# Kernel optimization log

Hardware: AMD Instinct MI355X
Metric: run time of the kernel (lower is better)

Reference implementation:

```python
import jax, jax.numpy as jnp
import numpy as np
import math

B_SZ, N, D, H = 16384, 10, 256, 8
D_H = D // H

def setup_inputs() -> dict:
    key = jax.random.key(0)
    ks = jax.random.split(key, 7)
    s = 1.0 / math.sqrt(D)
    return {
        "Z": jax.random.normal(ks[0], (B_SZ, N, D), dtype=jnp.float32),
        "role_pos_ids": jax.random.randint(ks[1], (B_SZ, N), 0, 10),
        "WQ": jax.random.normal(ks[2], (D, D), dtype=jnp.float32) * s,
        "WK": jax.random.normal(ks[3], (D, D), dtype=jnp.float32) * s,
        "WV": jax.random.normal(ks[4], (D, D), dtype=jnp.float32) * s,
        "WO": jax.random.normal(ks[5], (D, D), dtype=jnp.float32) * s,
        "Bp": jax.random.normal(ks[6], (H, 10, 10), dtype=jnp.float32) * 0.02,
    }

def reference(Z, role_pos_ids, WQ, WK, WV, WO, Bp):
    Bs, n, _ = Z.shape
    # projections -> (B, H, N, d_h)
    q = (Z @ WQ).reshape(Bs, n, H, D_H).transpose(0, 2, 1, 3)
    k = (Z @ WK).reshape(Bs, n, H, D_H).transpose(0, 2, 1, 3)
    v = (Z @ WV).reshape(Bs, n, H, D_H).transpose(0, 2, 1, 3)
    scores = jnp.einsum('bhid,bhjd->bhij', q, k) / math.sqrt(D_H)
    # bias[b,h,i,j] = Bp[h, c[b,i], c[b,j]]  -> advanced indexing gives (H,B,N,N)
    bias = Bp[:, role_pos_ids[:, :, None], role_pos_ids[:, None, :]]
    scores = scores + bias.transpose(1, 0, 2, 3)
    attn = jax.nn.softmax(scores, axis=-1)
    out = jnp.einsum('bhij,bhjd->bhid', attn, v)
    out = out.transpose(0, 2, 1, 3).reshape(Bs, n, D)
    return out @ WO
```

## Files before the change

kernel.cpp:

```cpp
#include <hip/hip_runtime.h>
#include <hip/hip_bf16.h>


typedef __attribute__((ext_vector_type(8))) short bf16x8;
typedef __attribute__((ext_vector_type(4))) float f32x4;

__device__ __forceinline__ unsigned short f2bf(float f) {
  union { __hip_bfloat16 h; unsigned short u; } cv;
  cv.h = __float2bfloat16(f);
  return cv.u;
}
__device__ __forceinline__ float bflo(unsigned int u) { return __uint_as_float(u << 16); }
__device__ __forceinline__ float bfhi(unsigned int u) { return __uint_as_float(u & 0xffff0000u); }

__global__ void prep_wt_kernel(const float* __restrict__ WQ, const float* __restrict__ WK,
                               const float* __restrict__ WV, const float* __restrict__ WO,
                               __hip_bfloat16* __restrict__ wt) {
  const int k = blockIdx.x;
  const int n = threadIdx.x;
  wt[0 * 65536 + n * 256 + k] = __float2bfloat16(WQ[k * 256 + n]);
  wt[1 * 65536 + n * 256 + k] = __float2bfloat16(WK[k * 256 + n]);
  wt[2 * 65536 + n * 256 + k] = __float2bfloat16(WV[k * 256 + n]);
  wt[3 * 65536 + n * 256 + k] = __float2bfloat16(WO[k * 256 + n]);
}

__global__ __launch_bounds__(256) void fused_qkv_attn_kernel(
    const float* __restrict__ Z, const __hip_bfloat16* __restrict__ wt,
    const int* __restrict__ roles, const float* __restrict__ Bp,
    __hip_bfloat16* __restrict__ attn_out, int gb_off)
{
  __shared__ __align__(16) char lds[72960];
  char* As = lds;
  char* Sp = lds + 40960;

  const int t = threadIdx.x;
  const int lane = t & 63;
  const int wv = t >> 6;
  const int g = lane >> 4, cx = lane & 15;
  const int blk = blockIdx.x;
  const size_t r0 = (size_t)blk * 80;

  #pragma unroll
  for (int c = 0; c < 10; ++c) {
    const int idx = c * 256 + t;
    const int row = idx >> 5, ch = idx & 31;
    const float* src = Z + (r0 + row) * 256 + ch * 8;
    float4 f0 = *(const float4*)(src);
    float4 f1 = *(const float4*)(src + 4);
    union { bf16x8 v; unsigned short u[8]; } pk;
    pk.u[0] = f2bf(f0.x); pk.u[1] = f2bf(f0.y);
    pk.u[2] = f2bf(f0.z); pk.u[3] = f2bf(f0.w);
    pk.u[4] = f2bf(f1.x); pk.u[5] = f2bf(f1.y);
    pk.u[6] = f2bf(f1.z); pk.u[7] = f2bf(f1.w);
    *(bf16x8*)(As + row * 512 + ((ch ^ (row & 7)) * 16)) = pk.v;
  }
  __syncthreads();

  #pragma unroll 1
  for (int p = 0; p < 4; ++p) {
    f32x4 acc[5][3];
    #pragma unroll
    for (int mi = 0; mi < 5; ++mi)
      #pragma unroll
      for (int nf = 0; nf < 3; ++nf) acc[mi][nf] = (f32x4){0.f, 0.f, 0.f, 0.f};

    const __hip_bfloat16* bptr[3];
    #pragma unroll
    for (int nf = 0; nf < 3; ++nf) {
      const int f = wv * 3 + nf;
      const int mf = f >> 2;
      const int ncol = p * 64 + (f & 3) * 16;
      bptr[nf] = wt + mf * 65536 + (ncol + cx) * 256 + g * 8;
    }
    #pragma unroll
    for (int kk = 0; kk < 8; ++kk) {
      bf16x8 bfr[3];
      #pragma unroll
      for (int nf = 0; nf < 3; ++nf) bfr[nf] = *(const bf16x8*)(bptr[nf] + kk * 32);
      bf16x8 afr[5];
      #pragma unroll
      for (int mi = 0; mi < 5; ++mi) {
        const int row = mi * 16 + cx;
        const int ch = (kk * 4 + g) ^ (row & 7);
        afr[mi] = *(const bf16x8*)(As + row * 512 + ch * 16);
      }
      #pragma unroll
      for (int mi = 0; mi < 5; ++mi)
        #pragma unroll
        for (int nf = 0; nf < 3; ++nf)
          acc[mi][nf] = __builtin_amdgcn_mfma_f32_16x16x32_bf16(afr[mi], bfr[nf], acc[mi][nf], 0, 0, 0);
    }
    #pragma unroll
    for (int mi = 0; mi < 5; ++mi)
      #pragma unroll
      for (int nf = 0; nf < 3; ++nf)
        #pragma unroll
        for (int jj = 0; jj < 4; ++jj) {
          const int row = mi * 16 + g * 4 + jj;
          const int col = wv * 48 + nf * 16 + cx;
          *(unsigned short*)(Sp + row * 400 + col * 2) = f2bf(acc[mi][nf][jj]);
        }
    __syncthreads();

    if (t < 160) {
      const int b = t / 20;
      const int hh = (t / 10) % 2;
      const int i = t % 10;
      const int h = 2 * p + hh;
      const int gb = gb_off + blk * 8 + b;
      const char* base = Sp + (b * 10) * 400 + hh * 64;

      float qf[32];
      {
        const char* qrow = base + i * 400;
        #pragma unroll
        for (int c = 0; c < 4; ++c) {
          uint4 u = *(const uint4*)(qrow + c * 16);
          qf[c*8+0] = bflo(u.x); qf[c*8+1] = bfhi(u.x);
          qf[c*8+2] = bflo(u.y); qf[c*8+3] = bfhi(u.y);
          qf[c*8+4] = bflo(u.z); qf[c*8+5] = bfhi(u.z);
          qf[c*8+6] = bflo(u.w); qf[c*8+7] = bfhi(u.w);
        }
      }
      const int ri = roles[gb * 10 + i];
      const float* bias_row = Bp + h * 100 + ri * 10;

      float s[10];
      #pragma unroll
      for (int j = 0; j < 10; ++j) {
        const char* krow = base + j * 400 + 128;
        float a = 0.f;
        #pragma unroll
        for (int c = 0; c < 4; ++c) {
          uint4 u = *(const uint4*)(krow + c * 16);
          a += qf[c*8+0]*bflo(u.x) + qf[c*8+1]*bfhi(u.x)
             + qf[c*8+2]*bflo(u.y) + qf[c*8+3]*bfhi(u.y)
             + qf[c*8+4]*bflo(u.z) + qf[c*8+5]*bfhi(u.z)
             + qf[c*8+6]*bflo(u.w) + qf[c*8+7]*bfhi(u.w);
        }
        const int rj = roles[gb * 10 + j];
        s[j] = a * 0.17677669529663687f + bias_row[rj];
      }
      float mx = s[0];
      #pragma unroll
      for (int j = 1; j < 10; ++j) mx = fmaxf(mx, s[j]);
      float pr[10], sum = 0.f;
      #pragma unroll
      for (int j = 0; j < 10; ++j) { pr[j] = expf(s[j] - mx); sum += pr[j]; }
      const float inv = 1.f / sum;

      float o[32];
      #pragma unroll
      for (int d = 0; d < 32; ++d) o[d] = 0.f;
      #pragma unroll
      for (int j = 0; j < 10; ++j) {
        const float pj = pr[j] * inv;
        const char* vrow = base + j * 400 + 256;
        #pragma unroll
        for (int c = 0; c < 4; ++c) {
          uint4 u = *(const uint4*)(vrow + c * 16);
          o[c*8+0] += pj * bflo(u.x); o[c*8+1] += pj * bfhi(u.x);
          o[c*8+2] += pj * bflo(u.y); o[c*8+3] += pj * bfhi(u.y);
          o[c*8+4] += pj * bflo(u.z); o[c*8+5] += pj * bfhi(u.z);
          o[c*8+6] += pj * bflo(u.w); o[c*8+7] += pj * bfhi(u.w);
        }
      }
      uint4* op = (uint4*)(attn_out + (r0 + b * 10 + i) * 256 + h * 32);
      #pragma unroll
      for (int c = 0; c < 4; ++c) {
        uint4 u;
        u.x = (unsigned)f2bf(o[c*8+0]) | ((unsigned)f2bf(o[c*8+1]) << 16);
        u.y = (unsigned)f2bf(o[c*8+2]) | ((unsigned)f2bf(o[c*8+3]) << 16);
        u.z = (unsigned)f2bf(o[c*8+4]) | ((unsigned)f2bf(o[c*8+5]) << 16);
        u.w = (unsigned)f2bf(o[c*8+6]) | ((unsigned)f2bf(o[c*8+7]) << 16);
        op[c] = u;
      }
    }
    __syncthreads();
  }
}

__global__ __launch_bounds__(256) void gemm_wo2_kernel(
    const __hip_bfloat16* __restrict__ A, const __hip_bfloat16* __restrict__ wt,
    float* __restrict__ C)
{
  __shared__ __align__(16) char As2[8192];
  const int t = threadIdx.x;
  const int lane = t & 63;
  const int wv = t >> 6;
  const int g = lane >> 4, cx = lane & 15;
  const size_t m0 = (size_t)blockIdx.x * 64;
  const __hip_bfloat16* WOT = wt + 3 * 65536;

  f32x4 acc[4][4];
  #pragma unroll
  for (int a = 0; a < 4; ++a)
    #pragma unroll
    for (int b = 0; b < 4; ++b) acc[a][b] = (f32x4){0.f, 0.f, 0.f, 0.f};

  #pragma unroll 1
  for (int ks = 0; ks < 4; ++ks) {
    if (ks) __syncthreads();
    #pragma unroll
    for (int c = 0; c < 2; ++c) {
      const int idx = c * 256 + t;
      const int row = idx >> 3, ch = idx & 7;
      uint4 raw = *(const uint4*)(A + (m0 + row) * 256 + ks * 64 + ch * 8);
      *(uint4*)(As2 + row * 128 + ((ch ^ (row & 7)) * 16)) = raw;
    }
    __syncthreads();
    #pragma unroll
    for (int kk = 0; kk < 2; ++kk) {
      bf16x8 bfr[4];
      #pragma unroll
      for (int nf = 0; nf < 4; ++nf) {
        const int n = wv * 64 + nf * 16 + cx;
        bfr[nf] = *(const bf16x8*)(WOT + n * 256 + ks * 64 + kk * 32 + g * 8);
      }
      bf16x8 afr[4];
      #pragma unroll
      for (int mi = 0; mi < 4; ++mi) {
        const int row = mi * 16 + cx;
        const int ch = (kk * 4 + g) ^ (row & 7);
        afr[mi] = *(const bf16x8*)(As2 + row * 128 + ch * 16);
      }
      #pragma unroll
      for (int mi = 0; mi < 4; ++mi)
        #pragma unroll
        for (int nf = 0; nf < 4; ++nf)
          acc[mi][nf] = __builtin_amdgcn_mfma_f32_16x16x32_bf16(afr[mi], bfr[nf], acc[mi][nf], 0, 0, 0);
    }
  }
  #pragma unroll
  for (int mi = 0; mi < 4; ++mi)
    #pragma unroll
    for (int nf = 0; nf < 4; ++nf)
      #pragma unroll
      for (int jj = 0; jj < 4; ++jj) {
        const size_t row = m0 + mi * 16 + g * 4 + jj;
        const int col = wv * 64 + nf * 16 + cx;
        C[row * 256 + col] = acc[mi][nf][jj];
      }
}

extern "C" void kernel_launch(void* const* d_in, const int* in_sizes, int n_in,
                              void* d_out, int out_size, void* d_ws, size_t ws_size,
                              hipStream_t stream)
{
  const float* Z     = (const float*)d_in[0];
  const int*   roles = (const int*)d_in[1];
  const float* WQ    = (const float*)d_in[2];
  const float* WK    = (const float*)d_in[3];
  const float* WV    = (const float*)d_in[4];
  const float* WO    = (const float*)d_in[5];
  const float* Bp    = (const float*)d_in[6];
  float* out = (float*)d_out;

  const long M = 163840;
  char* ws = (char*)d_ws;
  __hip_bfloat16* wt = (__hip_bfloat16*)ws;
  const size_t WT_BYTES = 4u * 256u * 256u * 2u;
  __hip_bfloat16* attn_ws = (__hip_bfloat16*)(ws + WT_BYTES);

  size_t avail = (ws_size > WT_BYTES) ? (ws_size - WT_BYTES) : 0;
  long rows_fit = (long)(avail / 512);
  long chunk = (rows_fit / 320) * 320;
  if (chunk > M) chunk = M;
  if (chunk < 320) chunk = 320;

  prep_wt_kernel<<<256, 256, 0, stream>>>(WQ, WK, WV, WO, wt);

  for (long r0 = 0; r0 < M; r0 += chunk) {
    long rows = M - r0;
    if (rows > chunk) rows = chunk;
    fused_qkv_attn_kernel<<<(int)(rows / 80), 256, 0, stream>>>(
        Z + r0 * 256, wt, roles, Bp, attn_ws, (int)(r0 / 10));
    gemm_wo2_kernel<<<(int)(rows / 64), 256, 0, stream>>>(
        attn_ws, wt, out + r0 * 256);
  }
}
```

Baseline: 252.5 us.

## Fuse output projection into attention kernel and overlap next-head QKV GEMM

Merges the separate WO GEMM into the fused QKV+attention kernel. Each head pair's attention output is written back into LDS and immediately multiplied by its slice of WO into persistent accumulators, so the bf16 attention intermediate never goes to global memory. The next head pair's QKV GEMM is issued before the attention step to overlap MFMA work with the scalar softmax code. Roles and Bp are staged in LDS and the score buffer is XOR-swizzled. The cost is higher register pressure from the extra 5x4 accumulator tile, under a launch bound requesting two blocks per CU with about 76 KB LDS each.

```diff
diff --git a/kernel.cpp b/kernel.cpp
--- a/kernel.cpp
+++ b/kernel.cpp
@@ -24,14 +24,16 @@
   wt[3 * 65536 + n * 256 + k] = __float2bfloat16(WO[k * 256 + n]);
 }
 
-__global__ __launch_bounds__(256) void fused_qkv_attn_kernel(
+__global__ __launch_bounds__(256, 2) void fused_all_kernel(
     const float* __restrict__ Z, const __hip_bfloat16* __restrict__ wt,
     const int* __restrict__ roles, const float* __restrict__ Bp,
-    __hip_bfloat16* __restrict__ attn_out, int gb_off)
+    float* __restrict__ out)
 {
-  __shared__ __align__(16) char lds[72960];
+  __shared__ __align__(16) char lds[76480];
   char* As = lds;
   char* Sp = lds + 40960;
+  int* roles_lds = (int*)(lds + 72960);
+  float* Bp_lds = (float*)(lds + 73280);
 
   const int t = threadIdx.x;
   const int lane = t & 63;
@@ -39,6 +41,9 @@
   const int g = lane >> 4, cx = lane & 15;
   const int blk = blockIdx.x;
   const size_t r0 = (size_t)blk * 80;
+
+  if (t < 80) roles_lds[t] = roles[r0 + t];
+  if (t < 200) ((float4*)Bp_lds)[t] = ((const float4*)Bp)[t];
 
   #pragma unroll
   for (int c = 0; c < 10; ++c) {
@@ -56,14 +61,18 @@
   }
   __syncthreads();
 
-  #pragma unroll 1
-  for (int p = 0; p < 4; ++p) {
-    f32x4 acc[5][3];
+  f32x4 acc_o[5][4];
+  #pragma unroll
+  for (int a = 0; a < 5; ++a)
+    #pragma unroll
+    for (int b = 0; b < 4; ++b) acc_o[a][b] = (f32x4){0.f, 0.f, 0.f, 0.f};
+  f32x4 acc_s[5][3];
+
+  auto gemm_qkv = [&](int p) {
     #pragma unroll
     for (int mi = 0; mi < 5; ++mi)
       #pragma unroll
-      for (int nf = 0; nf < 3; ++nf) acc[mi][nf] = (f32x4){0.f, 0.f, 0.f, 0.f};
-
+      for (int nf = 0; nf < 3; ++nf) acc_s[mi][nf] = (f32x4){0.f, 0.f, 0.f, 0.f};
     const __hip_bfloat16* bptr[3];
     #pragma unroll
     for (int nf = 0; nf < 3; ++nf) {
@@ -88,8 +97,11 @@
       for (int mi = 0; mi < 5; ++mi)
         #pragma unroll
         for (int nf = 0; nf < 3; ++nf)
-          acc[mi][nf] = __builtin_amdgcn_mfma_f32_16x16x32_bf16(afr[mi], bfr[nf], acc[mi][nf], 0, 0, 0);
-    }
+          acc_s[mi][nf] = __builtin_amdgcn_mfma_f32_16x16x32_bf16(afr[mi], bfr[nf], acc_s[mi][nf], 0, 0, 0);
+    }
+  };
+
+  auto epi = [&]() {
     #pragma unroll
     for (int mi = 0; mi < 5; ++mi)
       #pragma unroll
@@ -98,148 +110,125 @@
         for (int jj = 0; jj < 4; ++jj) {
           const int row = mi * 16 + g * 4 + jj;
           const int col = wv * 48 + nf * 16 + cx;
-          *(unsigned short*)(Sp + row * 400 + col * 2) = f2bf(acc[mi][nf][jj]);
+          const int region = col >> 6;
+          const int c = (col >> 3) & 7;
+          *(unsigned short*)(Sp + row * 400 + region * 128 +
+                             ((c ^ (row & 7)) * 16) + (col & 7) * 2) = f2bf(acc_s[mi][nf][jj]);
         }
-    __syncthreads();
-
-    if (t < 160) {
-      const int b = t / 20;
-      const int hh = (t / 10) % 2;
-      const int i = t % 10;
-      const int h = 2 * p + hh;
-      const int gb = gb_off + blk * 8 + b;
-      const char* base = Sp + (b * 10) * 400 + hh * 64;
-
-      float qf[32];
-      {
-        const char* qrow = base + i * 400;
-        #pragma unroll
-        for (int c = 0; c < 4; ++c) {
-          uint4 u = *(const uint4*)(qrow + c * 16);
-          qf[c*8+0] = bflo(u.x); qf[c*8+1] = bfhi(u.x);
-          qf[c*8+2] = bflo(u.y); qf[c*8+3] = bfhi(u.y);
-          qf[c*8+4] = bflo(u.z); qf[c*8+5] = bfhi(u.z);
-          qf[c*8+6] = bflo(u.w); qf[c*8+7] = bfhi(u.w);
-        }
-      }
-      const int ri = roles[gb * 10 + i];
-      const float* bias_row = Bp + h * 100 + ri * 10;
-
-      float s[10];
-      #pragma unroll
-      for (int j = 0; j < 10; ++j) {
-        const char* krow = base + j * 400 + 128;
-        float a = 0.f;
-        #pragma unroll
-        for (int c = 0; c < 4; ++c) {
-          uint4 u = *(const uint4*)(krow + c * 16);
-          a += qf[c*8+0]*bflo(u.x) + qf[c*8+1]*bfhi(u.x)
-             + qf[c*8+2]*bflo(u.y) + qf[c*8+3]*bfhi(u.y)
-             + qf[c*8+4]*bflo(u.z) + qf[c*8+5]*bfhi(u.z)
-             + qf[c*8+6]*bflo(u.w) + qf[c*8+7]*bfhi(u.w);
-        }
-        const int rj = roles[gb * 10 + j];
-        s[j] = a * 0.17677669529663687f + bias_row[rj];
-      }
-      float mx = s[0];
-      #pragma unroll
-      for (int j = 1; j < 10; ++j) mx = fmaxf(mx, s[j]);
-      float pr[10], sum = 0.f;
-      #pragma unroll
-      for (int j = 0; j < 10; ++j) { pr[j] = expf(s[j] - mx); sum += pr[j]; }
-      const float inv = 1.f / sum;
-
-      float o[32];
-      #pragma unroll
-      for (int d = 0; d < 32; ++d) o[d] = 0.f;
-      #pragma unroll
-      for (int j = 0; j < 10; ++j) {
-        const float pj = pr[j] * inv;
-        const char* vrow = base + j * 400 + 256;
-        #pragma unroll
-        for (int c = 0; c < 4; ++c) {
-          uint4 u = *(const uint4*)(vrow + c * 16);
-          o[c*8+0] += pj * bflo(u.x); o[c*8+1] += pj * bfhi(u.x);
-          o[c*8+2] += pj * bflo(u.y); o[c*8+3] += pj * bfhi(u.y);
-          o[c*8+4] += pj * bflo(u.z); o[c*8+5] += pj * bfhi(u.z);
-          o[c*8+6] += pj * bflo(u.w); o[c*8+7] += pj * bfhi(u.w);
-        }
-      }
-      uint4* op = (uint4*)(attn_out + (r0 + b * 10 + i) * 256 + h * 32);
+  };
+
+  auto attn = [&](int p) {
+    const int b = t / 20, hh = (t / 10) % 2, i = t % 10;
+    const int h = p * 2 + hh;
+    const int lrow = b * 10 + i;
+    float qf[32];
+    #pragma unroll
+    for (int c = 0; c < 4; ++c) {
+      uint4 u = *(const uint4*)(Sp + lrow * 400 + (((hh * 4 + c) ^ (lrow & 7)) * 16));
+      qf[c*8+0] = bflo(u.x); qf[c*8+1] = bfhi(u.x);
+      qf[c*8+2] = bflo(u.y); qf[c*8+3] = bfhi(u.y);
+      qf[c*8+4] = bflo(u.z); qf[c*8+5] = bfhi(u.z);
+      qf[c*8+6] = bflo(u.w); qf[c*8+7] = bfhi(u.w);
+    }
+    const int ri = roles_lds[b * 10 + i];
+    const float* brow = Bp_lds + h * 100 + ri * 10;
+    float s[10];
+    #pragma unroll
+    for (int j = 0; j < 10; ++j) {
+      const int kr = b * 10 + j;
+      const char* kbase = Sp + kr * 400 + 128;
+      float a = 0.f;
       #pragma unroll
       for (int c = 0; c < 4; ++c) {
-        uint4 u;
-        u.x = (unsigned)f2bf(o[c*8+0]) | ((unsigned)f2bf(o[c*8+1]) << 16);
-        u.y = (unsigned)f2bf(o[c*8+2]) | ((unsigned)f2bf(o[c*8+3]) << 16);
-        u.z = (unsigned)f2bf(o[c*8+4]) | ((unsigned)f2bf(o[c*8+5]) << 16);
-        u.w = (unsigned)f2bf(o[c*8+6]) | ((unsigned)f2bf(o[c*8+7]) << 16);
-        op[c] = u;
-      }
-    }
-    __syncthreads();
-  }
-}
-
-__global__ __launch_bounds__(256) void gemm_wo2_kernel(
-    const __hip_bfloat16* __restrict__ A, const __hip_bfloat16* __restrict__ wt,
-    float* __restrict__ C)
-{
-  __shared__ __align__(16) char As2[8192];
-  const int t = threadIdx.x;
-  const int lane = t & 63;
-  const int wv = t >> 6;
-  const int g = lane >> 4, cx = lane & 15;
-  const size_t m0 = (size_t)blockIdx.x * 64;
-  const __hip_bfloat16* WOT = wt + 3 * 65536;
-
-  f32x4 acc[4][4];
-  #pragma unroll
-  for (int a = 0; a < 4; ++a)
-    #pragma unroll
-    for (int b = 0; b < 4; ++b) acc[a][b] = (f32x4){0.f, 0.f, 0.f, 0.f};
-
-  #pragma unroll 1
-  for (int ks = 0; ks < 4; ++ks) {
-    if (ks) __syncthreads();
-    #pragma unroll
-    for (int c = 0; c < 2; ++c) {
-      const int idx = c * 256 + t;
-      const int row = idx >> 3, ch = idx & 7;
-      uint4 raw = *(const uint4*)(A + (m0 + row) * 256 + ks * 64 + ch * 8);
-      *(uint4*)(As2 + row * 128 + ((ch ^ (row & 7)) * 16)) = raw;
-    }
-    __syncthreads();
+        uint4 u = *(const uint4*)(kbase + (((hh * 4 + c) ^ (kr & 7)) * 16));
+        a += qf[c*8+0]*bflo(u.x) + qf[c*8+1]*bfhi(u.x)
+           + qf[c*8+2]*bflo(u.y) + qf[c*8+3]*bfhi(u.y)
+           + qf[c*8+4]*bflo(u.z) + qf[c*8+5]*bfhi(u.z)
+           + qf[c*8+6]*bflo(u.w) + qf[c*8+7]*bfhi(u.w);
+      }
+      s[j] = a * 0.17677669529663687f + brow[roles_lds[b * 10 + j]];
+    }
+    float mx = s[0];
+    #pragma unroll
+    for (int j = 1; j < 10; ++j) mx = fmaxf(mx, s[j]);
+    float pr[10], sum = 0.f;
+    #pragma unroll
+    for (int j = 0; j < 10; ++j) { pr[j] = expf(s[j] - mx); sum += pr[j]; }
+    const float inv = 1.f / sum;
+    float o[32];
+    #pragma unroll
+    for (int d = 0; d < 32; ++d) o[d] = 0.f;
+    #pragma unroll
+    for (int j = 0; j < 10; ++j) {
+      const float pj = pr[j] * inv;
+      const int kr = b * 10 + j;
+      const char* vbase = Sp + kr * 400 + 256;
+      #pragma unroll
+      for (int c = 0; c < 4; ++c) {
+        uint4 u = *(const uint4*)(vbase + (((hh * 4 + c) ^ (kr & 7)) * 16));
+        o[c*8+0] += pj * bflo(u.x); o[c*8+1] += pj * bfhi(u.x);
+        o[c*8+2] += pj * bflo(u.y); o[c*8+3] += pj * bfhi(u.y);
+        o[c*8+4] += pj * bflo(u.z); o[c*8+5] += pj * bfhi(u.z);
+        o[c*8+6] += pj * bflo(u.w); o[c*8+7] += pj * bfhi(u.w);
+      }
+    }
+    #pragma unroll
+    for (int c = 0; c < 4; ++c) {
+      uint4 u;
+      u.x = (unsigned)f2bf(o[c*8+0]) | ((unsigned)f2bf(o[c*8+1]) << 16);
+      u.y = (unsigned)f2bf(o[c*8+2]) | ((unsigned)f2bf(o[c*8+3]) << 16);
+      u.z = (unsigned)f2bf(o[c*8+4]) | ((unsigned)f2bf(o[c*8+5]) << 16);
+      u.w = (unsigned)f2bf(o[c*8+6]) | ((unsigned)f2bf(o[c*8+7]) << 16);
+      *(uint4*)(Sp + lrow * 400 + (((hh * 4 + c) ^ (lrow & 7)) * 16)) = u;
+    }
+  };
+
+  auto wo = [&](int p) {
+    const __hip_bfloat16* WOT = wt + 3 * 65536;
     #pragma unroll
     for (int kk = 0; kk < 2; ++kk) {
-      bf16x8 bfr[4];
+      bf16x8 bw[4];
       #pragma unroll
       for (int nf = 0; nf < 4; ++nf) {
         const int n = wv * 64 + nf * 16 + cx;
-        bfr[nf] = *(const bf16x8*)(WOT + n * 256 + ks * 64 + kk * 32 + g * 8);
-      }
-      bf16x8 afr[4];
-      #pragma unroll
-      for (int mi = 0; mi < 4; ++mi) {
+        bw[nf] = *(const bf16x8*)(WOT + n * 256 + p * 64 + kk * 32 + g * 8);
+      }
+      bf16x8 aw[5];
+      #pragma unroll
+      for (int mi = 0; mi < 5; ++mi) {
         const int row = mi * 16 + cx;
         const int ch = (kk * 4 + g) ^ (row & 7);
-        afr[mi] = *(const bf16x8*)(As2 + row * 128 + ch * 16);
-      }
-      #pragma unroll
-      for (int mi = 0; mi < 4; ++mi)
+        aw[mi] = *(const bf16x8*)(Sp + row * 400 + ch * 16);
+      }
+      #pragma unroll
+      for (int mi = 0; mi < 5; ++mi)
         #pragma unroll
         for (int nf = 0; nf < 4; ++nf)
-          acc[mi][nf] = __builtin_amdgcn_mfma_f32_16x16x32_bf16(afr[mi], bfr[nf], acc[mi][nf], 0, 0, 0);
-    }
+          acc_o[mi][nf] = __builtin_amdgcn_mfma_f32_16x16x32_bf16(aw[mi], bw[nf], acc_o[mi][nf], 0, 0, 0);
+    }
+  };
+
+  gemm_qkv(0);
+  #pragma unroll 1
+  for (int p = 0; p < 4; ++p) {
+    __syncthreads();
+    epi();
+    __syncthreads();
+    if (p < 3) gemm_qkv(p + 1);
+    if (t < 160) attn(p);
+    __syncthreads();
+    wo(p);
   }
+
   #pragma unroll
-  for (int mi = 0; mi < 4; ++mi)
+  for (int mi = 0; mi < 5; ++mi)
     #pragma unroll
     for (int nf = 0; nf < 4; ++nf)
       #pragma unroll
       for (int jj = 0; jj < 4; ++jj) {
-        const size_t row = m0 + mi * 16 + g * 4 + jj;
+        const size_t row = r0 + mi * 16 + g * 4 + jj;
         const int col = wv * 64 + nf * 16 + cx;
-        C[row * 256 + col] = acc[mi][nf][jj];
+        out[row * 256 + col] = acc_o[mi][nf][jj];
       }
 }
 
@@ -256,26 +245,8 @@
   const float* Bp    = (const float*)d_in[6];
   float* out = (float*)d_out;
 
-  const long M = 163840;
-  char* ws = (char*)d_ws;
-  __hip_bfloat16* wt = (__hip_bfloat16*)ws;
-  const size_t WT_BYTES = 4u * 256u * 256u * 2u;
-  __hip_bfloat16* attn_ws = (__hip_bfloat16*)(ws + WT_BYTES);
-
-  size_t avail = (ws_size > WT_BYTES) ? (ws_size - WT_BYTES) : 0;
-  long rows_fit = (long)(avail / 512);
-  long chunk = (rows_fit / 320) * 320;
-  if (chunk > M) chunk = M;
-  if (chunk < 320) chunk = 320;
+  __hip_bfloat16* wt = (__hip_bfloat16*)d_ws;
 
   prep_wt_kernel<<<256, 256, 0, stream>>>(WQ, WK, WV, WO, wt);
-
-  for (long r0 = 0; r0 < M; r0 += chunk) {
-    long rows = M - r0;
-    if (rows > chunk) rows = chunk;
-    fused_qkv_attn_kernel<<<(int)(rows / 80), 256, 0, stream>>>(
-        Z + r0 * 256, wt, roles, Bp, attn_ws, (int)(r0 / 10));
-    gemm_wo2_kernel<<<(int)(rows / 64), 256, 0, stream>>>(
-        attn_ws, wt, out + r0 * 256);
-  }
-}
+  fused_all_kernel<<<2048, 256, 0, stream>>>(Z, wt, roles, Bp, out);
+}
```

After: 439.9 us. +74.2%, slower.

## Halve attention block tile to 40 rows and swizzle QKV staging in LDS

Applied to the files above, without the earlier changes.

Each fused QKV+attention block now handles 4 batches (40 rows) instead of 8. This shrinks LDS from about 72KB to about 40KB, so with launch_bounds(256,4) more blocks can be resident per CU. The QKV staging buffer gets an XOR-swizzled layout to reduce bank conflicts, and roles are cached in LDS. Softmax uses __expf. The cost is that the 48-row MFMA tiling wastes rows 40-47, which read uninitialized LDS but are discarded, and per-row weight fetches double since each block reloads the weight fragments for half as many rows.

```diff
diff --git a/kernel.cpp b/kernel.cpp
--- a/kernel.cpp
+++ b/kernel.cpp
@@ -24,27 +24,32 @@
   wt[3 * 65536 + n * 256 + k] = __float2bfloat16(WO[k * 256 + n]);
 }
 
-__global__ __launch_bounds__(256) void fused_qkv_attn_kernel(
+#define AS_OFF 0
+#define SP_OFF 24576
+#define RL_OFF 40576
+#define LDS_SZ 40624
+
+__global__ __launch_bounds__(256, 4) void fused_qkv_attn_kernel(
     const float* __restrict__ Z, const __hip_bfloat16* __restrict__ wt,
     const int* __restrict__ roles, const float* __restrict__ Bp,
-    __hip_bfloat16* __restrict__ attn_out, int gb_off)
+    __hip_bfloat16* __restrict__ attn_out)
 {
-  __shared__ __align__(16) char lds[72960];
-  char* As = lds;
-  char* Sp = lds + 40960;
+  __shared__ __align__(16) char lds[LDS_SZ];
+  unsigned char* rl = (unsigned char*)(lds + RL_OFF);
 
   const int t = threadIdx.x;
   const int lane = t & 63;
   const int wv = t >> 6;
   const int g = lane >> 4, cx = lane & 15;
   const int blk = blockIdx.x;
-  const size_t r0 = (size_t)blk * 80;
-
+  const size_t c0 = (size_t)blk * 40;
+
+  if (t < 48) rl[t] = (t < 40) ? (unsigned char)roles[c0 + t] : 0;
   #pragma unroll
-  for (int c = 0; c < 10; ++c) {
+  for (int c = 0; c < 5; ++c) {
     const int idx = c * 256 + t;
     const int row = idx >> 5, ch = idx & 31;
-    const float* src = Z + (r0 + row) * 256 + ch * 8;
+    const float* src = Z + (c0 + row) * 256 + ch * 8;
     float4 f0 = *(const float4*)(src);
     float4 f1 = *(const float4*)(src + 4);
     union { bf16x8 v; unsigned short u[8]; } pk;
@@ -52,120 +57,118 @@
     pk.u[2] = f2bf(f0.z); pk.u[3] = f2bf(f0.w);
     pk.u[4] = f2bf(f1.x); pk.u[5] = f2bf(f1.y);
     pk.u[6] = f2bf(f1.z); pk.u[7] = f2bf(f1.w);
-    *(bf16x8*)(As + row * 512 + ((ch ^ (row & 7)) * 16)) = pk.v;
+    *(bf16x8*)(lds + AS_OFF + row * 512 + ((ch ^ (row & 7)) * 16)) = pk.v;
   }
   __syncthreads();
 
   #pragma unroll 1
   for (int p = 0; p < 4; ++p) {
-    f32x4 acc[5][3];
-    #pragma unroll
-    for (int mi = 0; mi < 5; ++mi)
-      #pragma unroll
-      for (int nf = 0; nf < 3; ++nf) acc[mi][nf] = (f32x4){0.f, 0.f, 0.f, 0.f};
-
-    const __hip_bfloat16* bptr[3];
-    #pragma unroll
-    for (int nf = 0; nf < 3; ++nf) {
-      const int f = wv * 3 + nf;
-      const int mf = f >> 2;
-      const int ncol = p * 64 + (f & 3) * 16;
-      bptr[nf] = wt + mf * 65536 + (ncol + cx) * 256 + g * 8;
-    }
-    #pragma unroll
-    for (int kk = 0; kk < 8; ++kk) {
-      bf16x8 bfr[3];
-      #pragma unroll
-      for (int nf = 0; nf < 3; ++nf) bfr[nf] = *(const bf16x8*)(bptr[nf] + kk * 32);
-      bf16x8 afr[5];
-      #pragma unroll
-      for (int mi = 0; mi < 5; ++mi) {
-        const int row = mi * 16 + cx;
-        const int ch = (kk * 4 + g) ^ (row & 7);
-        afr[mi] = *(const bf16x8*)(As + row * 512 + ch * 16);
-      }
-      #pragma unroll
-      for (int mi = 0; mi < 5; ++mi)
-        #pragma unroll
-        for (int nf = 0; nf < 3; ++nf)
-          acc[mi][nf] = __builtin_amdgcn_mfma_f32_16x16x32_bf16(afr[mi], bfr[nf], acc[mi][nf], 0, 0, 0);
-    }
-    #pragma unroll
-    for (int mi = 0; mi < 5; ++mi)
-      #pragma unroll
-      for (int nf = 0; nf < 3; ++nf)
+    f32x4 acc_s[3][3];
+    #pragma unroll
+    for (int mi = 0; mi < 3; ++mi)
+      #pragma unroll
+      for (int nf = 0; nf < 3; ++nf) acc_s[mi][nf] = (f32x4){0.f, 0.f, 0.f, 0.f};
+    {
+      const __hip_bfloat16* bptr[3];
+      #pragma unroll
+      for (int nf = 0; nf < 3; ++nf) {
+        const int f = wv * 3 + nf;
+        const int mf = f >> 2;
+        const int ncol = p * 64 + (f & 3) * 16;
+        bptr[nf] = wt + mf * 65536 + (ncol + cx) * 256 + g * 8;
+      }
+      #pragma unroll
+      for (int kk = 0; kk < 8; ++kk) {
+        bf16x8 bfr[3];
+        #pragma unroll
+        for (int nf = 0; nf < 3; ++nf) bfr[nf] = *(const bf16x8*)(bptr[nf] + kk * 32);
+        bf16x8 afr[3];
+        #pragma unroll
+        for (int mi = 0; mi < 3; ++mi) {
+          const int row = mi * 16 + cx;
+          const int ch = (kk * 4 + g) ^ (row & 7);
+          afr[mi] = *(const bf16x8*)(lds + AS_OFF + row * 512 + ch * 16);
+        }
+        #pragma unroll
+        for (int mi = 0; mi < 3; ++mi)
+          #pragma unroll
+          for (int nf = 0; nf < 3; ++nf)
+            acc_s[mi][nf] = __builtin_amdgcn_mfma_f32_16x16x32_bf16(afr[mi], bfr[nf], acc_s[mi][nf], 0, 0, 0);
+      }
+    }
+    #pragma unroll
+    for (int mi = 0; mi < 3; ++mi)
+      #pragma unroll
+      for (int nf = 0; nf < 3; ++nf) {
+        const int col = wv * 48 + nf * 16 + cx;
+        const int region = col >> 6;
+        const int cch = (col >> 3) & 7;
         #pragma unroll
         for (int jj = 0; jj < 4; ++jj) {
           const int row = mi * 16 + g * 4 + jj;
-          const int col = wv * 48 + nf * 16 + cx;
-          *(unsigned short*)(Sp + row * 400 + col * 2) = f2bf(acc[mi][nf][jj]);
-        }
+          if (row < 40)
+            *(unsigned short*)(lds + SP_OFF + row * 400 + region * 128 +
+                ((cch ^ (row & 7)) * 16) + (col & 7) * 2) = f2bf(acc_s[mi][nf][jj]);
+        }
+      }
     __syncthreads();
 
-    if (t < 160) {
-      const int b = t / 20;
-      const int hh = (t / 10) % 2;
-      const int i = t % 10;
-      const int h = 2 * p + hh;
-      const int gb = gb_off + blk * 8 + b;
-      const char* base = Sp + (b * 10) * 400 + hh * 64;
-
+    if (t < 80) {
+      const int b = t / 20, hh = (t / 10) % 2, i = t % 10;
+      const int h = p * 2 + hh;
+      const int lrow = b * 10 + i;
       float qf[32];
-      {
-        const char* qrow = base + i * 400;
+      #pragma unroll
+      for (int c = 0; c < 4; ++c) {
+        uint4 u = *(const uint4*)(lds + SP_OFF + lrow * 400 + (((hh * 4 + c) ^ (lrow & 7)) * 16));
+        qf[c*8+0] = bflo(u.x); qf[c*8+1] = bfhi(u.x);
+        qf[c*8+2] = bflo(u.y); qf[c*8+3] = bfhi(u.y);
+        qf[c*8+4] = bflo(u.z); qf[c*8+5] = bfhi(u.z);
+        qf[c*8+6] = bflo(u.w); qf[c*8+7] = bfhi(u.w);
+      }
+      const int ri = rl[lrow];
+      const float* brow = Bp + h * 100 + ri * 10;
+      float s[10];
+      #pragma unroll
+      for (int j = 0; j < 10; ++j) {
+        const int kr = b * 10 + j;
+        const char* kbase = lds + SP_OFF + kr * 400 + 128;
+        float a = 0.f;
         #pragma unroll
         for (int c = 0; c < 4; ++c) {
-          uint4 u = *(const uint4*)(qrow + c * 16);
-          qf[c*8+0] = bflo(u.x); qf[c*8+1] = bfhi(u.x);
-          qf[c*8+2] = bflo(u.y); qf[c*8+3] = bfhi(u.y);
-          qf[c*8+4] = bflo(u.z); qf[c*8+5] = bfhi(u.z);
-          qf[c*8+6] = bflo(u.w); qf[c*8+7] = bfhi(u.w);
-        }
-      }
-      const int ri = roles[gb * 10 + i];
-      const float* bias_row = Bp + h * 100 + ri * 10;
-
-      float s[10];
-      #pragma unroll
-      for (int j = 0; j < 10; ++j) {
-        const char* krow = base + j * 400 + 128;
-        float a = 0.f;
-        #pragma unroll
-        for (int c = 0; c < 4; ++c) {
-          uint4 u = *(const uint4*)(krow + c * 16);
+          uint4 u = *(const uint4*)(kbase + (((hh * 4 + c) ^ (kr & 7)) * 16));
           a += qf[c*8+0]*bflo(u.x) + qf[c*8+1]*bfhi(u.x)
              + qf[c*8+2]*bflo(u.y) + qf[c*8+3]*bfhi(u.y)
              + qf[c*8+4]*bflo(u.z) + qf[c*8+5]*bfhi(u.z)
              + qf[c*8+6]*bflo(u.w) + qf[c*8+7]*bfhi(u.w);
         }
-        const int rj = roles[gb * 10 + j];
-        s[j] = a * 0.17677669529663687f + bias_row[rj];
+        s[j] = a * 0.17677669529663687f + brow[rl[kr]];
       }
       float mx = s[0];
       #pragma unroll
       for (int j = 1; j < 10; ++j) mx = fmaxf(mx, s[j]);
-      float pr[10], sum = 0.f;
-      #pragma unroll
-      for (int j = 0; j < 10; ++j) { pr[j] = expf(s[j] - mx); sum += pr[j]; }
+      float sum = 0.f;
+      #pragma unroll
+      for (int j = 0; j < 10; ++j) { s[j] = __expf(s[j] - mx); sum += s[j]; }
       const float inv = 1.f / sum;
-
       float o[32];
       #pragma unroll
       for (int d = 0; d < 32; ++d) o[d] = 0.f;
       #pragma unroll
       for (int j = 0; j < 10; ++j) {
-        const float pj = pr[j] * inv;
-        const char* vrow = base + j * 400 + 256;
+        const float pj = s[j] * inv;
+        const int kr = b * 10 + j;
+        const char* vbase = lds + SP_OFF + kr * 400 + 256;
         #pragma unroll
         for (int c = 0; c < 4; ++c) {
-          uint4 u = *(const uint4*)(vrow + c * 16);
+          uint4 u = *(const uint4*)(vbase + (((hh * 4 + c) ^ (kr & 7)) * 16));
           o[c*8+0] += pj * bflo(u.x); o[c*8+1] += pj * bfhi(u.x);
           o[c*8+2] += pj * bflo(u.y); o[c*8+3] += pj * bfhi(u.y);
           o[c*8+4] += pj * bflo(u.z); o[c*8+5] += pj * bfhi(u.z);
           o[c*8+6] += pj * bflo(u.w); o[c*8+7] += pj * bfhi(u.w);
         }
       }
-      uint4* op = (uint4*)(attn_out + (r0 + b * 10 + i) * 256 + h * 32);
+      uint4* op = (uint4*)(attn_out + (c0 + lrow) * 256 + h * 32);
       #pragma unroll
       for (int c = 0; c < 4; ++c) {
         uint4 u;
@@ -273,8 +276,8 @@
   for (long r0 = 0; r0 < M; r0 += chunk) {
     long rows = M - r0;
     if (rows > chunk) rows = chunk;
-    fused_qkv_attn_kernel<<<(int)(rows / 80), 256, 0, stream>>>(
-        Z + r0 * 256, wt, roles, Bp, attn_ws, (int)(r0 / 10));
+    fused_qkv_attn_kernel<<<(int)(rows / 40), 256, 0, stream>>>(
+        Z + r0 * 256, wt, roles + r0, Bp, attn_ws);
     gemm_wo2_kernel<<<(int)(rows / 64), 256, 0, stream>>>(
         attn_ws, wt, out + r0 * 256);
   }
```

After: 754.2 us. +198.6%, slower.
